# Kernel tuning notes

Measured on AMD Instinct MI355X. Metric: run time of the kernel, lower is better.

Reference implementation:

```python
import jax, jax.numpy as jnp
import numpy as np

N_NODES = 4096
N_EDGES = 262144
D = 128
N_REL = 1000
N_ENT = 50000


def setup_inputs() -> dict:
    key = jax.random.key(0)
    ks = jax.random.split(key, 6)
    x = jax.random.normal(ks[0], (N_NODES, D), dtype=jnp.float32)
    edge_index = jax.random.randint(ks[1], (2, N_EDGES), 0, N_NODES)
    relation_id = jax.random.randint(ks[2], (N_EDGES,), 0, N_REL)
    neg_flag = jax.random.randint(ks[3], (N_EDGES,), 0, 2)
    rel_emb = jax.random.normal(ks[4], (N_REL, D), dtype=jnp.float32)
    entity_emb = jax.random.normal(ks[5], (N_ENT, D), dtype=jnp.float32)
    scale = jnp.ones((N_ENT,), dtype=jnp.float32)
    bias = jnp.zeros((N_ENT,), dtype=jnp.float32)
    return {"x": x, "edge_index": edge_index, "relation_id": relation_id,
            "neg_flag": neg_flag, "rel_emb": rel_emb, "entity_emb": entity_emb,
            "scale": scale, "bias": bias}


def reference(x, edge_index, relation_id, neg_flag, rel_emb, entity_emb, scale, bias):
    src, dst = edge_index[0], edge_index[1]
    # message: gather x_j, TransE tail estimate, sign flip for negated atoms
    neg_coef = 1.0 - 2.0 * neg_flag.astype(x.dtype)           # [E]
    msg = (x[src] + rel_emb[relation_id]) * neg_coef[:, None]  # [E, D]
    # aggregate: scatter-add into target nodes
    aggr_out = jax.ops.segment_sum(msg, dst, num_segments=x.shape[0])  # [N, D]
    # update: residual + bias/scale double-matmul through entity table
    aggr = 0.1 * x + aggr_out                                  # [N, D]
    entity_score = aggr @ entity_emb.T                          # [N, V]
    entity_score = jax.nn.relu(entity_score * scale + bias)
    out = entity_score @ entity_emb                             # [N, D]
    return out
```

## Files before the change

### kernel.cpp

```cpp
#include <hip/hip_runtime.h>
#include <stdint.h>

typedef __attribute__((ext_vector_type(8))) short short8;
typedef __attribute__((ext_vector_type(8))) unsigned short ushort8;
typedef __attribute__((ext_vector_type(4))) float f32x4;

#define NNODES 4096
#define NEDGES 262144
#define DIM 128
#define NENT 50000
#define NENTP 50048
#define NTILES 782
#define NSPLIT 16
#define CHUNK 49

__device__ __forceinline__ unsigned short f2bf(float f) {
  union { __bf16 b; unsigned short u; } c;
  c.b = (__bf16)f;
  return c.u;
}

__global__ __launch_bounds__(256) void k_hist(
    const int* __restrict__ ei, int* __restrict__ cnt)
{
  int e = blockIdx.x * 256 + threadIdx.x;
  atomicAdd(&cnt[ei[NEDGES + e]], 1);
}

__global__ __launch_bounds__(1024) void k_scan(
    const int* __restrict__ cnt, int* __restrict__ off, int* __restrict__ cur)
{
  __shared__ int s[1024];
  int t = threadIdx.x;
  int4 v = reinterpret_cast<const int4*>(cnt)[t];
  int lsum = v.x + v.y + v.z + v.w;
  s[t] = lsum; __syncthreads();
  for (int d = 1; d < 1024; d <<= 1) {
    int a = (t >= d) ? s[t - d] : 0;
    __syncthreads();
    s[t] += a;
    __syncthreads();
  }
  int base = s[t] - lsum;
  int4 o; o.x = base; o.y = base + v.x; o.z = o.y + v.y; o.w = o.z + v.z;
  reinterpret_cast<int4*>(off)[t] = o;
  reinterpret_cast<int4*>(cur)[t] = o;
  if (t == 1023) off[4096] = base + lsum;
}

__global__ __launch_bounds__(256) void k_place(
    const int* __restrict__ ei, const int* __restrict__ rid,
    const int* __restrict__ nf, int* __restrict__ cur, int* __restrict__ sorted)
{
  int e = blockIdx.x * 256 + threadIdx.x;
  int dst = ei[NEDGES + e];
  int pos = atomicAdd(&cur[dst], 1);
  sorted[pos] = ei[e] | (rid[e] << 12) | (nf[e] << 22);
}

__global__ __launch_bounds__(256) void k_aggr(
    const int* __restrict__ off, const int* __restrict__ sorted,
    const float* __restrict__ x, const float* __restrict__ rel,
    unsigned short* __restrict__ q)
{
  __shared__ float sAcc[8 * 132];
  const int n = blockIdx.x;
  const int t = threadIdx.x;
  const int slot = t >> 5;
  const int c = t & 31;
  const int b = off[n], eN = off[n + 1];
  float4 acc = make_float4(0.f, 0.f, 0.f, 0.f);
  for (int i = b + slot; i < eN; i += 8) {
    int p = sorted[i];
    float4 xv = reinterpret_cast<const float4*>(x)[(p & 4095) * 32 + c];
    float4 rv = reinterpret_cast<const float4*>(rel)[((p >> 12) & 1023) * 32 + c];
    float sgn = (p & (1 << 22)) ? -1.f : 1.f;
    acc.x += sgn * (xv.x + rv.x);
    acc.y += sgn * (xv.y + rv.y);
    acc.z += sgn * (xv.z + rv.z);
    acc.w += sgn * (xv.w + rv.w);
  }
  *reinterpret_cast<float4*>(&sAcc[slot * 132 + c * 4]) = acc;
  __syncthreads();
  if (t < 128) {
    float s = 0.f;
#pragma unroll
    for (int k = 0; k < 8; ++k) s += sAcc[k * 132 + t];
    q[n * DIM + t] = f2bf(0.1f * x[n * DIM + t] + s);
  }
}

__global__ __launch_bounds__(256) void k_prep(
    const float* __restrict__ ent, const float* __restrict__ scale,
    unsigned short* __restrict__ ebf, unsigned short* __restrict__ etbf)
{
  __shared__ float sT[64 * 133];
  const int t = threadIdx.x;
  const int e0 = blockIdx.x * 64;
#pragma unroll
  for (int i = 0; i < 8; ++i) {
    int idx = i * 256 + t;
    int e = idx >> 5;
    int c4 = idx & 31;
    float4 v = make_float4(0.f, 0.f, 0.f, 0.f);
    float sc = 0.f;
    if (e0 + e < NENT) {
      v = reinterpret_cast<const float4*>(ent)[(e0 + e) * 32 + c4];
      sc = scale[e0 + e];
    }
    *reinterpret_cast<float4*>(&sT[e * 133 + c4 * 4]) = v;
    ushort4 bq;
    bq.x = f2bf(v.x * sc); bq.y = f2bf(v.y * sc);
    bq.z = f2bf(v.z * sc); bq.w = f2bf(v.w * sc);
    *reinterpret_cast<ushort4*>(&ebf[(e0 + e) * 128 + c4 * 4]) = bq;
  }
  __syncthreads();
  const int lane = t & 63;
  const int w = t >> 6;
  const int dl = lane >> 3;
  const int el = (lane & 7) * 8;
#pragma unroll
  for (int it = 0; it < 4; ++it) {
    int d = it * 32 + w * 8 + dl;
    ushort8 buf;
#pragma unroll
    for (int j = 0; j < 8; ++j) buf[j] = f2bf(sT[(el + j) * 133 + d]);
    *reinterpret_cast<ushort8*>(&etbf[d * NENTP + e0 + el]) = buf;
  }
}

__global__ __launch_bounds__(512, 4) void k_flash(
    const unsigned short* __restrict__ qg,
    const unsigned short* __restrict__ ebf,
    const unsigned short* __restrict__ etbf,
    const float* __restrict__ bias,
    float* __restrict__ out)
{
  __shared__ __align__(16) unsigned short sE[64 * 136];
  __shared__ __align__(16) unsigned short sET[128 * 72];
  __shared__ __align__(16) unsigned short sP[128 * 72];
  __shared__ float sBias[64];

  const int t = threadIdx.x;
  const int lane = t & 63;
  const int w = t >> 6;
  const int wm = w >> 1;
  const int wn = w & 1;
  const int l15 = lane & 15;
  const int quad = lane >> 4;

  const int m0 = blockIdx.x * 128;
  const int tile_lo = blockIdx.y * CHUNK;
  const int tile_hi = (tile_lo + CHUNK < NTILES) ? (tile_lo + CHUNK) : NTILES;

  const int vA0 = t >> 4,          chA0 = t & 15;
  const int vA1 = (512 + t) >> 4,  chA1 = t & 15;
  const int dT0 = t >> 3,          chT0 = t & 7;
  const int dT1 = (512 + t) >> 3,  chT1 = t & 7;

  short8 qf[2][4];
  for (int h = 0; h < 2; ++h) {
#pragma unroll
    for (int i = 0; i < 2; ++i) {
      int idx = i * 512 + t;
      int v = idx >> 4, ch = idx & 15;
      uint4 val = reinterpret_cast<const uint4*>(qg)[(m0 + h * 64 + v) * 16 + ch];
      *reinterpret_cast<uint4*>(&sET[v * 136 + ch * 8]) = val;
    }
    __syncthreads();
    if ((wm >> 1) == h) {
      int lr = (wm & 1) * 32;
#pragma unroll
      for (int tm = 0; tm < 2; ++tm)
#pragma unroll
        for (int kk = 0; kk < 4; ++kk)
          qf[tm][kk] = *reinterpret_cast<const short8*>(
              &sET[(lr + tm * 16 + l15) * 136 + kk * 32 + quad * 8]);
    }
    __syncthreads();
  }

  f32x4 accO[2][4];
#pragma unroll
  for (int tm = 0; tm < 2; ++tm)
#pragma unroll
    for (int td = 0; td < 4; ++td) accO[tm][td] = {0.f, 0.f, 0.f, 0.f};

  uint4 rE0, rE1, rT0, rT1;
  float rB;
  {
    const int vt0 = tile_lo * 64;
    rE0 = *reinterpret_cast<const uint4*>(&ebf[(vt0 + vA0) * 128 + chA0 * 8]);
    rE1 = *reinterpret_cast<const uint4*>(&ebf[(vt0 + vA1) * 128 + chA1 * 8]);
    rT0 = *reinterpret_cast<const uint4*>(&etbf[dT0 * NENTP + vt0 + chT0 * 8]);
    rT1 = *reinterpret_cast<const uint4*>(&etbf[dT1 * NENTP + vt0 + chT1 * 8]);
    rB = (t < 64 && vt0 + t < NENT) ? bias[vt0 + t] : 0.f;
  }

  for (int tile = tile_lo; tile < tile_hi; ++tile) {
    *reinterpret_cast<uint4*>(&sE[vA0 * 136 + chA0 * 8]) = rE0;
    *reinterpret_cast<uint4*>(&sE[vA1 * 136 + chA1 * 8]) = rE1;
    *reinterpret_cast<uint4*>(&sET[dT0 * 72 + chT0 * 8]) = rT0;
    *reinterpret_cast<uint4*>(&sET[dT1 * 72 + chT1 * 8]) = rT1;
    if (t < 64) sBias[t] = rB;
    __syncthreads();

    if (tile + 1 < tile_hi) {
      const int vt0n = (tile + 1) * 64;
      rE0 = *reinterpret_cast<const uint4*>(&ebf[(vt0n + vA0) * 128 + chA0 * 8]);
      rE1 = *reinterpret_cast<const uint4*>(&ebf[(vt0n + vA1) * 128 + chA1 * 8]);
      rT0 = *reinterpret_cast<const uint4*>(&etbf[dT0 * NENTP + vt0n + chT0 * 8]);
      rT1 = *reinterpret_cast<const uint4*>(&etbf[dT1 * NENTP + vt0n + chT1 * 8]);
      rB = (t < 64 && vt0n + t < NENT) ? bias[vt0n + t] : 0.f;
    }

    f32x4 accS[2][2];
#pragma unroll
    for (int tm = 0; tm < 2; ++tm)
#pragma unroll
      for (int tn = 0; tn < 2; ++tn) accS[tm][tn] = {0.f, 0.f, 0.f, 0.f};
#pragma unroll
    for (int kk = 0; kk < 4; ++kk) {
      short8 bE[2];
#pragma unroll
      for (int tn = 0; tn < 2; ++tn)
        bE[tn] = *reinterpret_cast<const short8*>(
            &sE[(wn * 32 + tn * 16 + l15) * 136 + kk * 32 + quad * 8]);
#pragma unroll
      for (int tm = 0; tm < 2; ++tm)
#pragma unroll
        for (int tn = 0; tn < 2; ++tn)
          accS[tm][tn] = __builtin_amdgcn_mfma_f32_16x16x32_bf16(
              qf[tm][kk], bE[tn], accS[tm][tn], 0, 0, 0);
    }

#pragma unroll
    for (int tm = 0; tm < 2; ++tm)
#pragma unroll
      for (int tn = 0; tn < 2; ++tn) {
        int col = wn * 32 + tn * 16 + l15;
        float bs = sBias[col];
#pragma unroll
        for (int r = 0; r < 4; ++r) {
          int row = wm * 32 + tm * 16 + quad * 4 + r;
          sP[row * 72 + col] = f2bf(fmaxf(accS[tm][tn][r] + bs, 0.f));
        }
      }
    __syncthreads();

#pragma unroll
    for (int kk = 0; kk < 2; ++kk) {
      short8 aP[2], bT[4];
#pragma unroll
      for (int tm = 0; tm < 2; ++tm)
        aP[tm] = *reinterpret_cast<const short8*>(
            &sP[(wm * 32 + tm * 16 + l15) * 72 + kk * 32 + quad * 8]);
#pragma unroll
      for (int td = 0; td < 4; ++td)
        bT[td] = *reinterpret_cast<const short8*>(
            &sET[(wn * 64 + td * 16 + l15) * 72 + kk * 32 + quad * 8]);
#pragma unroll
      for (int tm = 0; tm < 2; ++tm)
#pragma unroll
        for (int td = 0; td < 4; ++td)
          accO[tm][td] = __builtin_amdgcn_mfma_f32_16x16x32_bf16(
              aP[tm], bT[td], accO[tm][td], 0, 0, 0);
    }
    __syncthreads();
  }

#pragma unroll
  for (int tm = 0; tm < 2; ++tm)
#pragma unroll
    for (int td = 0; td < 4; ++td)
#pragma unroll
      for (int r = 0; r < 4; ++r) {
        int row = m0 + wm * 32 + tm * 16 + quad * 4 + r;
        int col = wn * 64 + td * 16 + l15;
        atomicAdd(&out[row * DIM + col], accO[tm][td][r]);
      }
}

extern "C" void kernel_launch(void* const* d_in, const int* in_sizes, int n_in,
                              void* d_out, int out_size, void* d_ws, size_t ws_size,
                              hipStream_t stream) {
  const float* x     = (const float*)d_in[0];
  const int*   ei    = (const int*)d_in[1];
  const int*   rid   = (const int*)d_in[2];
  const int*   nf    = (const int*)d_in[3];
  const float* rel   = (const float*)d_in[4];
  const float* ent   = (const float*)d_in[5];
  const float* scale = (const float*)d_in[6];
  const float* bias  = (const float*)d_in[7];
  float* out = (float*)d_out;

  char* ws = (char*)d_ws;
  int*            cnt    = (int*)(ws + 0);
  int*            off    = (int*)(ws + (16u << 10));
  int*            cur    = (int*)(ws + (36u << 10));
  int*            sorted = (int*)(ws + (64u << 10));
  unsigned short* qb     = (unsigned short*)(ws + (1344u << 10));
  unsigned short* ebf    = (unsigned short*)(ws + (2560u << 10));
  unsigned short* etbf   = (unsigned short*)(ws + (2560u << 10) + (size_t)NENTP * DIM * 2);

  hipMemsetAsync(cnt, 0, 4096 * sizeof(int), stream);
  hipMemsetAsync(d_out, 0, (size_t)out_size * sizeof(float), stream);
  k_prep<<<NTILES, 256, 0, stream>>>(ent, scale, ebf, etbf);
  k_hist<<<NEDGES / 256, 256, 0, stream>>>(ei, cnt);
  k_scan<<<1, 1024, 0, stream>>>(cnt, off, cur);
  k_place<<<NEDGES / 256, 256, 0, stream>>>(ei, rid, nf, cur, sorted);
  k_aggr<<<NNODES, 256, 0, stream>>>(off, sorted, x, rel, qb);
  k_flash<<<dim3(NNODES / 128, NSPLIT), 512, 0, stream>>>(qb, ebf, etbf, bias, out);
}
```

Measured before the change: 282.9 us.

## Rewrite flash kernel with 32x32 MFMA, LDS double-buffering via global_load_lds, register-resident P

```diff
diff --git a/kernel.cpp b/kernel.cpp
--- a/kernel.cpp
+++ b/kernel.cpp
@@ -4,6 +4,8 @@
 typedef __attribute__((ext_vector_type(8))) short short8;
 typedef __attribute__((ext_vector_type(8))) unsigned short ushort8;
 typedef __attribute__((ext_vector_type(4))) float f32x4;
+typedef __attribute__((ext_vector_type(16))) float f32x16;
+typedef __attribute__((ext_vector_type(2))) unsigned int uint2v;
 
 #define NNODES 4096
 #define NEDGES 262144
@@ -129,156 +131,156 @@
   }
 }
 
-__global__ __launch_bounds__(512, 4) void k_flash(
+
+__device__ __forceinline__ void gll16(const void* g, void* l) {
+  __builtin_amdgcn_global_load_lds(
+      (const __attribute__((address_space(1))) unsigned int*)g,
+      (__attribute__((address_space(3))) unsigned int*)l, 16, 0, 0);
+}
+
+__device__ __forceinline__ unsigned cvtpk(float lo, float hi) {
+  unsigned r;
+  asm("v_cvt_pk_bf16_f32 %0, %1, %2" : "=v"(r) : "v"(lo), "v"(hi));
+  return r;
+}
+
+__global__ __launch_bounds__(256, 2) void k_flash(
     const unsigned short* __restrict__ qg,
     const unsigned short* __restrict__ ebf,
     const unsigned short* __restrict__ etbf,
     const float* __restrict__ bias,
     float* __restrict__ out)
 {
-  __shared__ __align__(16) unsigned short sE[64 * 136];
-  __shared__ __align__(16) unsigned short sET[128 * 72];
-  __shared__ __align__(16) unsigned short sP[128 * 72];
-  __shared__ float sBias[64];
+  __shared__ __align__(16) unsigned short sE[2][64 * 128];
+  __shared__ __align__(16) unsigned short sET[2][128 * 64];
+  __shared__ __align__(16) float sBias[2][64];
 
   const int t = threadIdx.x;
+  const int w = t >> 6;
   const int lane = t & 63;
-  const int w = t >> 6;
-  const int wm = w >> 1;
-  const int wn = w & 1;
-  const int l15 = lane & 15;
-  const int quad = lane >> 4;
+  const int l31 = lane & 31;
+  const int hi = lane >> 5;
 
   const int m0 = blockIdx.x * 128;
   const int tile_lo = blockIdx.y * CHUNK;
   const int tile_hi = (tile_lo + CHUNK < NTILES) ? (tile_lo + CHUNK) : NTILES;
 
-  const int vA0 = t >> 4,          chA0 = t & 15;
-  const int vA1 = (512 + t) >> 4,  chA1 = t & 15;
-  const int dT0 = t >> 3,          chT0 = t & 7;
-  const int dT1 = (512 + t) >> 3,  chT1 = t & 7;
-
-  short8 qf[2][4];
-  for (int h = 0; h < 2; ++h) {
-#pragma unroll
-    for (int i = 0; i < 2; ++i) {
-      int idx = i * 512 + t;
-      int v = idx >> 4, ch = idx & 15;
-      uint4 val = reinterpret_cast<const uint4*>(qg)[(m0 + h * 64 + v) * 16 + ch];
-      *reinterpret_cast<uint4*>(&sET[v * 136 + ch * 8]) = val;
-    }
+  const int cE = (((t & 15) ^ ((t >> 4) & 15))) * 8;
+  const int rE = (t >> 4) & 15;
+  const int cT = (((t & 7) ^ ((t >> 3) & 7))) * 8;
+  const int rT = t >> 3;
+
+  short8 qf[8];
+  {
+    const unsigned short* qrow = qg + (size_t)(m0 + w * 32 + l31) * DIM + hi * 8;
+#pragma unroll
+    for (int kk = 0; kk < 8; ++kk)
+      qf[kk] = *reinterpret_cast<const short8*>(qrow + kk * 16);
+  }
+
+  f32x16 accO[4];
+#pragma unroll
+  for (int td = 0; td < 4; ++td)
+#pragma unroll
+    for (int r = 0; r < 16; ++r) accO[td][r] = 0.f;
+
+  {
+    const int vt = tile_lo * 64;
+#pragma unroll
+    for (int i = 0; i < 4; ++i)
+      gll16(ebf + (size_t)(vt + i * 16 + rE) * DIM + cE, &sE[0][i * 2048 + w * 512]);
+#pragma unroll
+    for (int i = 0; i < 4; ++i)
+      gll16(etbf + (size_t)(i * 32 + rT) * NENTP + vt + cT, &sET[0][i * 2048 + w * 512]);
+    if (t < 64) sBias[0][t] = (vt + t < NENT) ? bias[vt + t] : 0.f;
+  }
+  __syncthreads();
+
+  int cur = 0;
+  for (int tile = tile_lo; tile < tile_hi; ++tile) {
+    if (tile + 1 < tile_hi) {
+      const int vt = (tile + 1) * 64;
+#pragma unroll
+      for (int i = 0; i < 4; ++i)
+        gll16(ebf + (size_t)(vt + i * 16 + rE) * DIM + cE, &sE[cur ^ 1][i * 2048 + w * 512]);
+#pragma unroll
+      for (int i = 0; i < 4; ++i)
+        gll16(etbf + (size_t)(i * 32 + rT) * NENTP + vt + cT, &sET[cur ^ 1][i * 2048 + w * 512]);
+      if (t < 64) sBias[cur ^ 1][t] = (vt + t < NENT) ? bias[vt + t] : 0.f;
+    }
+
+    f32x16 accST[2];
+#pragma unroll
+    for (int te = 0; te < 2; ++te)
+#pragma unroll
+      for (int r = 0; r < 16; ++r) accST[te][r] = 0.f;
+
+    const unsigned short* sEc = sE[cur];
+    __builtin_amdgcn_s_setprio(1);
+#pragma unroll
+    for (int kk = 0; kk < 8; ++kk) {
+      const int col = ((kk * 2 + hi) ^ (l31 & 15)) * 8;
+      short8 a0 = *reinterpret_cast<const short8*>(&sEc[l31 * 128 + col]);
+      short8 a1 = *reinterpret_cast<const short8*>(&sEc[(32 + l31) * 128 + col]);
+      accST[0] = __builtin_amdgcn_mfma_f32_32x32x16_bf16(a0, qf[kk], accST[0], 0, 0, 0);
+      accST[1] = __builtin_amdgcn_mfma_f32_32x32x16_bf16(a1, qf[kk], accST[1], 0, 0, 0);
+    }
+    __builtin_amdgcn_s_setprio(0);
+
+    short8 F[4];
+    const float* sb = sBias[cur];
+#pragma unroll
+    for (int te = 0; te < 2; ++te) {
+      float p[16];
+#pragma unroll
+      for (int g = 0; g < 4; ++g) {
+        f32x4 b4 = *reinterpret_cast<const f32x4*>(&sb[te * 32 + g * 8 + hi * 4]);
+#pragma unroll
+        for (int j = 0; j < 4; ++j)
+          p[g * 4 + j] = fmaxf(accST[te][g * 4 + j] + b4[j], 0.f);
+      }
+      unsigned wr[8];
+#pragma unroll
+      for (int c2 = 0; c2 < 8; ++c2) wr[c2] = cvtpk(p[2 * c2], p[2 * c2 + 1]);
+      uint2v r02 = __builtin_amdgcn_permlane32_swap(wr[0], wr[2], false, false);
+      uint2v r13 = __builtin_amdgcn_permlane32_swap(wr[1], wr[3], false, false);
+      uint2v r46 = __builtin_amdgcn_permlane32_swap(wr[4], wr[6], false, false);
+      uint2v r57 = __builtin_amdgcn_permlane32_swap(wr[5], wr[7], false, false);
+      union { unsigned u[4]; short8 s; } f0, f1;
+      f0.u[0] = r02[0]; f0.u[1] = r13[0]; f0.u[2] = r02[1]; f0.u[3] = r13[1];
+      f1.u[0] = r46[0]; f1.u[1] = r57[0]; f1.u[2] = r46[1]; f1.u[3] = r57[1];
+      F[te * 2 + 0] = f0.s;
+      F[te * 2 + 1] = f1.s;
+    }
+
+    const unsigned short* sTc = sET[cur];
+    __builtin_amdgcn_s_setprio(1);
+#pragma unroll
+    for (int ke = 0; ke < 4; ++ke) {
+#pragma unroll
+      for (int td = 0; td < 4; ++td) {
+        const int d = td * 32 + l31;
+        const int col = ((ke * 2 + hi) ^ (l31 & 7)) * 8;
+        short8 bT = *reinterpret_cast<const short8*>(&sTc[d * 64 + col]);
+        accO[td] = __builtin_amdgcn_mfma_f32_32x32x16_bf16(F[ke], bT, accO[td], 0, 0, 0);
+      }
+    }
+    __builtin_amdgcn_s_setprio(0);
+
     __syncthreads();
-    if ((wm >> 1) == h) {
-      int lr = (wm & 1) * 32;
-#pragma unroll
-      for (int tm = 0; tm < 2; ++tm)
-#pragma unroll
-        for (int kk = 0; kk < 4; ++kk)
-          qf[tm][kk] = *reinterpret_cast<const short8*>(
-              &sET[(lr + tm * 16 + l15) * 136 + kk * 32 + quad * 8]);
-    }
-    __syncthreads();
-  }
-
-  f32x4 accO[2][4];
-#pragma unroll
-  for (int tm = 0; tm < 2; ++tm)
-#pragma unroll
-    for (int td = 0; td < 4; ++td) accO[tm][td] = {0.f, 0.f, 0.f, 0.f};
-
-  uint4 rE0, rE1, rT0, rT1;
-  float rB;
-  {
-    const int vt0 = tile_lo * 64;
-    rE0 = *reinterpret_cast<const uint4*>(&ebf[(vt0 + vA0) * 128 + chA0 * 8]);
-    rE1 = *reinterpret_cast<const uint4*>(&ebf[(vt0 + vA1) * 128 + chA1 * 8]);
-    rT0 = *reinterpret_cast<const uint4*>(&etbf[dT0 * NENTP + vt0 + chT0 * 8]);
-    rT1 = *reinterpret_cast<const uint4*>(&etbf[dT1 * NENTP + vt0 + chT1 * 8]);
-    rB = (t < 64 && vt0 + t < NENT) ? bias[vt0 + t] : 0.f;
-  }
-
-  for (int tile = tile_lo; tile < tile_hi; ++tile) {
-    *reinterpret_cast<uint4*>(&sE[vA0 * 136 + chA0 * 8]) = rE0;
-    *reinterpret_cast<uint4*>(&sE[vA1 * 136 + chA1 * 8]) = rE1;
-    *reinterpret_cast<uint4*>(&sET[dT0 * 72 + chT0 * 8]) = rT0;
-    *reinterpret_cast<uint4*>(&sET[dT1 * 72 + chT1 * 8]) = rT1;
-    if (t < 64) sBias[t] = rB;
-    __syncthreads();
-
-    if (tile + 1 < tile_hi) {
-      const int vt0n = (tile + 1) * 64;
-      rE0 = *reinterpret_cast<const uint4*>(&ebf[(vt0n + vA0) * 128 + chA0 * 8]);
-      rE1 = *reinterpret_cast<const uint4*>(&ebf[(vt0n + vA1) * 128 + chA1 * 8]);
-      rT0 = *reinterpret_cast<const uint4*>(&etbf[dT0 * NENTP + vt0n + chT0 * 8]);
-      rT1 = *reinterpret_cast<const uint4*>(&etbf[dT1 * NENTP + vt0n + chT1 * 8]);
-      rB = (t < 64 && vt0n + t < NENT) ? bias[vt0n + t] : 0.f;
-    }
-
-    f32x4 accS[2][2];
-#pragma unroll
-    for (int tm = 0; tm < 2; ++tm)
-#pragma unroll
-      for (int tn = 0; tn < 2; ++tn) accS[tm][tn] = {0.f, 0.f, 0.f, 0.f};
-#pragma unroll
-    for (int kk = 0; kk < 4; ++kk) {
-      short8 bE[2];
-#pragma unroll
-      for (int tn = 0; tn < 2; ++tn)
-        bE[tn] = *reinterpret_cast<const short8*>(
-            &sE[(wn * 32 + tn * 16 + l15) * 136 + kk * 32 + quad * 8]);
-#pragma unroll
-      for (int tm = 0; tm < 2; ++tm)
-#pragma unroll
-        for (int tn = 0; tn < 2; ++tn)
-          accS[tm][tn] = __builtin_amdgcn_mfma_f32_16x16x32_bf16(
-              qf[tm][kk], bE[tn], accS[tm][tn], 0, 0, 0);
-    }
-
-#pragma unroll
-    for (int tm = 0; tm < 2; ++tm)
-#pragma unroll
-      for (int tn = 0; tn < 2; ++tn) {
-        int col = wn * 32 + tn * 16 + l15;
-        float bs = sBias[col];
-#pragma unroll
-        for (int r = 0; r < 4; ++r) {
-          int row = wm * 32 + tm * 16 + quad * 4 + r;
-          sP[row * 72 + col] = f2bf(fmaxf(accS[tm][tn][r] + bs, 0.f));
-        }
-      }
-    __syncthreads();
-
-#pragma unroll
-    for (int kk = 0; kk < 2; ++kk) {
-      short8 aP[2], bT[4];
-#pragma unroll
-      for (int tm = 0; tm < 2; ++tm)
-        aP[tm] = *reinterpret_cast<const short8*>(
-            &sP[(wm * 32 + tm * 16 + l15) * 72 + kk * 32 + quad * 8]);
-#pragma unroll
-      for (int td = 0; td < 4; ++td)
-        bT[td] = *reinterpret_cast<const short8*>(
-            &sET[(wn * 64 + td * 16 + l15) * 72 + kk * 32 + quad * 8]);
-#pragma unroll
-      for (int tm = 0; tm < 2; ++tm)
-#pragma unroll
-        for (int td = 0; td < 4; ++td)
-          accO[tm][td] = __builtin_amdgcn_mfma_f32_16x16x32_bf16(
-              aP[tm], bT[td], accO[tm][td], 0, 0, 0);
-    }
-    __syncthreads();
-  }
-
-#pragma unroll
-  for (int tm = 0; tm < 2; ++tm)
-#pragma unroll
-    for (int td = 0; td < 4; ++td)
-#pragma unroll
-      for (int r = 0; r < 4; ++r) {
-        int row = m0 + wm * 32 + tm * 16 + quad * 4 + r;
-        int col = wn * 64 + td * 16 + l15;
-        atomicAdd(&out[row * DIM + col], accO[tm][td][r]);
-      }
+    cur ^= 1;
+  }
+
+#pragma unroll
+  for (int td = 0; td < 4; ++td) {
+#pragma unroll
+    for (int r = 0; r < 16; ++r) {
+      int qrow = (r & 3) + 8 * (r >> 2) + 4 * hi;
+      int row = m0 + w * 32 + qrow;
+      int col = td * 32 + l31;
+      atomicAdd(&out[(size_t)row * DIM + col], accO[td][r]);
+    }
+  }
 }
 
 extern "C" void kernel_launch(void* const* d_in, const int* in_sizes, int n_in,
@@ -310,5 +312,5 @@
   k_scan<<<1, 1024, 0, stream>>>(cnt, off, cur);
   k_place<<<NEDGES / 256, 256, 0, stream>>>(ei, rid, nf, cur, sorted);
   k_aggr<<<NNODES, 256, 0, stream>>>(off, sorted, x, rel, qb);
-  k_flash<<<dim3(NNODES / 128, NSPLIT), 512, 0, stream>>>(qb, ebf, etbf, bias, out);
-}
+  k_flash<<<dim3(NNODES / 128, NSPLIT), 256, 0, stream>>>(qb, ebf, etbf, bias, out);
+}
```

Measured after the change: 276.4 us. -2.3%, faster.
